# Performance work log

Hardware: AMD Instinct MI355X
Metric: run time of the kernel (lower is better)

## Reference

```python
import jax, jax.numpy as jnp
import numpy as np

N = 20000
DEG = 16
E = N * DEG
IN_DIM = 512
OUT_DIM = 512
H = 4
D = OUT_DIM // H            # head_dim = 128
POS_DIM = 3
M_ROPE = D // (POS_DIM * 2) # 21
D_ROPE = POS_DIM * 2 * M_ROPE  # 126 (2 trailing dims unrotated)
ROPE_BASE = 10000.0

INV_FREQ = jnp.exp(-jnp.arange(M_ROPE, dtype=jnp.float32) * (np.log(ROPE_BASE) / M_ROPE))


def _rope(t, pos):
    # t: (N, D, H), pos: (N, POS_DIM)
    n = t.shape[0]
    angles = pos[:, :, None] * INV_FREQ[None, None, :]        # (N, POS_DIM, M)
    cos = jnp.cos(angles)[..., None]                           # (N, POS_DIM, M, 1)
    sin = jnp.sin(angles)[..., None]
    part = t[:, :D_ROPE, :].reshape(n, POS_DIM, M_ROPE, 2, H)
    even, odd = part[..., 0, :], part[..., 1, :]
    rot_even = even * cos - odd * sin
    rot_odd = even * sin + odd * cos
    rot = jnp.stack((rot_even, rot_odd), axis=3).reshape(n, D_ROPE, H)
    return jnp.concatenate([rot, t[:, D_ROPE:, :]], axis=1)


def setup_inputs() -> dict:
    key = jax.random.key(0)
    ks = jax.random.split(key, 12)
    x = jax.random.normal(ks[0], (N, IN_DIM), jnp.float32)
    pos = jax.random.uniform(ks[1], (N, POS_DIM), jnp.float32) * 100.0
    rows = jnp.repeat(jnp.arange(N, dtype=jnp.int32), DEG)  # sorted, every node has DEG out-edges
    cols = jax.random.randint(ks[2], (E,), 0, N, dtype=jnp.int32)
    s = 1.0 / np.sqrt(IN_DIM)
    Wq = jax.random.normal(ks[3], (OUT_DIM, IN_DIM), jnp.float32) * s
    Wk = jax.random.normal(ks[4], (OUT_DIM, IN_DIM), jnp.float32) * s
    Wv = jax.random.normal(ks[5], (OUT_DIM, IN_DIM), jnp.float32) * s
    Wo = jax.random.normal(ks[6], (OUT_DIM, OUT_DIM), jnp.float32) * s
    bq = jax.random.normal(ks[7], (OUT_DIM,), jnp.float32) * 0.01
    bk = jax.random.normal(ks[8], (OUT_DIM,), jnp.float32) * 0.01
    bv = jax.random.normal(ks[9], (OUT_DIM,), jnp.float32) * 0.01
    bo = jax.random.normal(ks[10], (OUT_DIM,), jnp.float32) * 0.01
    return {"x": x, "pos": pos, "rows": rows, "cols": cols,
            "Wq": Wq, "bq": bq, "Wk": Wk, "bk": bk, "Wv": Wv, "bv": bv, "Wo": Wo, "bo": bo}


def reference(x, pos, rows, cols, Wq, bq, Wk, bk, Wv, bv, Wo, bo):
    n = x.shape[0]
    q = (x @ Wq.T + bq).reshape(n, D, H)
    k = (x @ Wk.T + bk).reshape(n, D, H)
    v = (x @ Wv.T + bv).reshape(n, D, H)
    # scaling by sqrt(k.size(1)) == sqrt(head_dim)
    q = q / jnp.sqrt(jnp.asarray(D, q.dtype))
    q = _rope(q, pos)
    k = _rope(k, pos)
    # per-edge scores: s[e,h] = sum_d q[rows[e],d,h] * k[cols[e],d,h]
    scores = jnp.einsum('edh,edh->eh', q[rows], k[cols])  # (E, H)
    # row-wise sparse softmax per head
    row_max = jax.ops.segment_max(scores, rows, num_segments=n, indices_are_sorted=True)
    p = jnp.exp(scores - row_max[rows])
    denom = jax.ops.segment_sum(p, rows, num_segments=n, indices_are_sorted=True)
    attn = p / denom[rows]                                 # (E, H)
    # bspmm: y[i,d,h] = sum_{e: rows[e]=i} attn[e,h] * v[cols[e],d,h]
    y = jax.ops.segment_sum(attn[:, None, :] * v[cols], rows, num_segments=n, indices_are_sorted=True)
    out = y.reshape(n, OUT_DIM) @ Wo.T + bo
    return out
```

## Files before the change

### kernel.cpp

```cpp
#include <hip/hip_runtime.h>
#include <hip/hip_bf16.h>

#define NN 20000
#define DEG 16
#define KD 512
#define OD 512
#define NH 4
#define DH 128
#define DROPE 126

#define BM 128
#define BN 128

typedef unsigned short u16;
typedef unsigned int u32;
typedef __attribute__((ext_vector_type(8))) short short8;
typedef __attribute__((ext_vector_type(4))) float f32x4;

__device__ __forceinline__ float b2f(u16 u){ return __uint_as_float((u32)u << 16); }
__device__ __forceinline__ u16 f2b(float f){
  u32 x = __float_as_uint(f);
  return (u16)((x + 0x7fffu + ((x >> 16) & 1u)) >> 16);
}
__device__ __forceinline__ void up8(uint4 u, float* f){
  f[0]=__uint_as_float(u.x<<16); f[1]=__uint_as_float(u.x&0xffff0000u);
  f[2]=__uint_as_float(u.y<<16); f[3]=__uint_as_float(u.y&0xffff0000u);
  f[4]=__uint_as_float(u.z<<16); f[5]=__uint_as_float(u.z&0xffff0000u);
  f[6]=__uint_as_float(u.w<<16); f[7]=__uint_as_float(u.w&0xffff0000u);
}
__device__ __forceinline__ uint4 cvt8(const float* s){
  uint4 a = *(const uint4*)s;
  uint4 b = *(const uint4*)(s + 4);
  uint4 o;
  o.x = (u32)f2b(__uint_as_float(a.x)) | ((u32)f2b(__uint_as_float(a.y)) << 16);
  o.y = (u32)f2b(__uint_as_float(a.z)) | ((u32)f2b(__uint_as_float(a.w)) << 16);
  o.z = (u32)f2b(__uint_as_float(b.x)) | ((u32)f2b(__uint_as_float(b.y)) << 16);
  o.w = (u32)f2b(__uint_as_float(b.z)) | ((u32)f2b(__uint_as_float(b.w)) << 16);
  return o;
}

__device__ __forceinline__ void load_lds16(const u16* g, u16* l) {
  __builtin_amdgcn_global_load_lds(
      (const __attribute__((address_space(1))) void*)g,
      (__attribute__((address_space(3))) void*)l, 16, 0, 0);
}

struct ConvJob {
  const float* x;  u16* xb;
  const float* w[4]; u16* wb[4];
  const float* b[4]; u16* bb[4];
};
__global__ __launch_bounds__(256) void conv_all(ConvJob j) {
  const int b = blockIdx.x;
  if (b < 5000) {
    const int i8 = (b * 256 + threadIdx.x) * 8;
    *(uint4*)(j.xb + i8) = cvt8(j.x + i8);
  } else if (b < 5512) {
    const int t = b - 5000;
    const int wsel = t >> 7;
    const int i8 = ((t & 127) * 256 + threadIdx.x) * 8;
    if (wsel < 3) {
      *(uint4*)(j.wb[wsel] + i8) = cvt8(j.w[wsel] + i8);
    } else {
      const int o = i8 >> 9, cp = i8 & 511;
      const int h = cp >> 7, d0 = cp & 127;
      const float* src = j.w[3] + (size_t)o * 512 + h;
      float tmp[8];
      #pragma unroll
      for (int t2 = 0; t2 < 8; t2++) tmp[t2] = src[(size_t)(d0 + t2) * 4];
      uint4 ov;
      ov.x = (u32)f2b(tmp[0]) | ((u32)f2b(tmp[1]) << 16);
      ov.y = (u32)f2b(tmp[2]) | ((u32)f2b(tmp[3]) << 16);
      ov.z = (u32)f2b(tmp[4]) | ((u32)f2b(tmp[5]) << 16);
      ov.w = (u32)f2b(tmp[6]) | ((u32)f2b(tmp[7]) << 16);
      *(uint4*)(j.wb[3] + i8) = ov;
    }
  } else {
    const int vsel = threadIdx.x >> 6;
    const int i8 = (threadIdx.x & 63) * 8;
    *(uint4*)(j.bb[vsel] + i8) = cvt8(j.b[vsel] + i8);
  }
}

#define BN2 256
__global__ __launch_bounds__(512, 4) void gemm_k(
    const u16* __restrict__ A,
    const u16* __restrict__ W0, const u16* __restrict__ B0,
    const u16* __restrict__ W1, const u16* __restrict__ B1,
    const u16* __restrict__ W2, const u16* __restrict__ B2,
    const float* __restrict__ pos,
    u16* __restrict__ o0, u16* __restrict__ o1, u16* __restrict__ o2,
    int M)
{
  __shared__ __align__(16) char smem[69632];
  __shared__ float posS[BM*3];
  __shared__ float freqS[21];
  u16* As = (u16*)smem;
  u16* Bs = As + BM*64;

  const int b = blockIdx.x;
  const int xcd = b & 7, rem = b >> 3;
  const int rowT = (rem / 6)*8 + xcd;
  const int sub = rem % 6;
  const int colT = sub & 1, w = sub >> 1;
  if (rowT*BM >= M) return;

  const int tid = threadIdx.x;
  const int wave = tid >> 6, lane = tid & 63;
  const int wr = wave >> 2, wc = wave & 3;
  const int lm = lane & 15, lq = lane >> 4;
  const u16* W  = (w == 0) ? W0 : ((w == 1) ? W1 : W2);
  const u16* Bi = (w == 0) ? B0 : ((w == 1) ? B1 : B2);
  const int emode = w;
  u16* outQKV = (w == 0) ? o0 : ((w == 1) ? o1 : o2);

  f32x4 acc[4][4];
  #pragma unroll
  for (int i = 0; i < 4; i++)
    #pragma unroll
    for (int jj = 0; jj < 4; jj++)
      acc[i][jj] = (f32x4){0.f, 0.f, 0.f, 0.f};

  if (emode < 2) {
    if (tid < BM) {
      int gr = rowT*BM + tid; if (gr >= M) gr = M - 1;
      posS[tid*3+0] = pos[gr*3+0];
      posS[tid*3+1] = pos[gr*3+1];
      posS[tid*3+2] = pos[gr*3+2];
    }
    if (tid >= BM && tid < BM + 21)
      freqS[tid - BM] = __expf(-(float)(tid - BM) * 0.43858763676077064f);
  }

  for (int kt = 0; kt < KD; kt += 64) {
    #pragma unroll
    for (int it = 0; it < 2; it++) {
      const int chunk = it*512 + tid;
      const int row = chunk >> 3, gseg = (chunk & 7) ^ (row & 7);
      int gr = rowT*BM + row; if (gr >= M) gr = M - 1;
      load_lds16(A + (size_t)gr*KD + kt + gseg*8,
                 As + (size_t)(it*512 + wave*64)*8);
    }
    #pragma unroll
    for (int it = 0; it < 4; it++) {
      const int chunk = it*512 + tid;
      const int row = chunk >> 3, gseg = (chunk & 7) ^ (row & 7);
      load_lds16(W + (size_t)(colT*BN2 + row)*KD + kt + gseg*8,
                 Bs + (size_t)(it*512 + wave*64)*8);
    }
    __syncthreads();
    #pragma unroll
    for (int kk = 0; kk < 64; kk += 32) {
      const int ks = kk >> 3;
      short8 af[4], bfr[4];
      #pragma unroll
      for (int i = 0; i < 4; i++) {
        const int ra = wr*64 + i*16 + lm;
        af[i] = *(const short8*)(As + (size_t)(ra*8 + ((ks + lq) ^ (ra & 7)))*8);
      }
      #pragma unroll
      for (int i = 0; i < 4; i++) {
        const int rb = wc*64 + i*16 + lm;
        bfr[i] = *(const short8*)(Bs + (size_t)(rb*8 + ((ks + lq) ^ (rb & 7)))*8);
      }
      #pragma unroll
      for (int mi = 0; mi < 4; mi++)
        #pragma unroll
        for (int ni = 0; ni < 4; ni++)
          acc[mi][ni] = __builtin_amdgcn_mfma_f32_16x16x32_bf16(af[mi], bfr[ni], acc[mi][ni], 0, 0, 0);
    }
    __syncthreads();
  }

  float bvv[4];
  #pragma unroll
  for (int ni = 0; ni < 4; ni++)
    bvv[ni] = b2f(Bi[colT*BN2 + wc*64 + ni*16 + lm]);

  u16* Cs = (u16*)smem;

  #pragma unroll
  for (int mi = 0; mi < 4; mi++) {
    #pragma unroll
    for (int ni = 0; ni < 4; ni++) {
      const int cloc = wc*64 + ni*16 + lm;
      const int h = cloc & 3, dloc = cloc >> 2;
      const int d = colT*64 + dloc;
      #pragma unroll
      for (int r = 0; r < 4; r++) {
        const int rloc = wr*64 + mi*16 + lq*4 + r;
        float v = acc[mi][ni][r] + bvv[ni];
        if (emode == 0) v *= 0.08838834764831845f;
        float vr = v;
        if (emode < 2) {
          const float partner = __shfl_xor(v, 4);
          if (d < DROPE) {
            const int pp = d / 42, rem2 = d - pp*42, m = rem2 >> 1, par = rem2 & 1;
            const float ang = posS[rloc*3 + pp] * freqS[m];
            float sn, cs; __sincosf(ang, &sn, &cs);
            vr = par ? (v*cs + partner*sn) : (v*cs - partner*sn);
          }
        }
        Cs[rloc*272 + h*68 + dloc] = f2b(vr);
      }
    }
  }
  __syncthreads();
  #pragma unroll
  for (int pass = 0; pass < 8; pass++) {
    const int c2 = pass*512 + tid;
    const int dd8 = c2 & 7, h = (c2 >> 3) & 3, rloc = c2 >> 5;
    const int grow = rowT*BM + rloc;
    if (grow < M) {
      uint2 a = *(const uint2*)(Cs + rloc*272 + h*68 + dd8*8);
      uint2 b2 = *(const uint2*)(Cs + rloc*272 + h*68 + dd8*8 + 4);
      *(uint4*)(outQKV + ((size_t)grow*NH + h)*DH + colT*64 + dd8*8)
          = make_uint4(a.x, a.y, b2.x, b2.y);
    }
  }
}

__global__ __launch_bounds__(256, 4) void gemm_o(
    const u16* __restrict__ A, const u16* __restrict__ W,
    const u16* __restrict__ Bi, float* __restrict__ out, int M)
{
  __shared__ __align__(16) u16 As[BM*64];
  __shared__ __align__(16) u16 Bs[BN*64];

  const int b = blockIdx.x;
  const int xcd = b & 7, rem = b >> 3;
  const int rowT = (rem >> 2)*8 + xcd, colT = rem & 3;
  if (rowT*BM >= M) return;

  const int tid = threadIdx.x;
  const int wave = tid >> 6, lane = tid & 63;
  const int wr = wave >> 1, wc = wave & 1;
  const int lm = lane & 15, lq = lane >> 4;

  f32x4 acc[4][4];
  #pragma unroll
  for (int i = 0; i < 4; i++)
    #pragma unroll
    for (int jj = 0; jj < 4; jj++)
      acc[i][jj] = (f32x4){0.f, 0.f, 0.f, 0.f};

  for (int kt = 0; kt < KD; kt += 64) {
    #pragma unroll
    for (int it = 0; it < 4; it++) {
      const int chunk = it*256 + wave*64 + lane;
      const int row = chunk >> 3, gseg = (chunk & 7) ^ (row & 7);
      int gr = rowT*BM + row; if (gr >= M) gr = M - 1;
      load_lds16(A + (size_t)gr*KD + kt + gseg*8,
                 As + (size_t)(it*256 + wave*64)*8);
    }
    #pragma unroll
    for (int it = 0; it < 4; it++) {
      const int chunk = it*256 + wave*64 + lane;
      const int row = chunk >> 3, gseg = (chunk & 7) ^ (row & 7);
      load_lds16(W + (size_t)(colT*BN + row)*KD + kt + gseg*8,
                 Bs + (size_t)(it*256 + wave*64)*8);
    }
    __syncthreads();
    #pragma unroll
    for (int kk = 0; kk < 64; kk += 32) {
      const int ks = kk >> 3;
      short8 af[4], bfr[4];
      #pragma unroll
      for (int i = 0; i < 4; i++) {
        const int ra = wr*64 + i*16 + lm;
        af[i] = *(const short8*)(As + (size_t)(ra*8 + ((ks + lq) ^ (ra & 7)))*8);
      }
      #pragma unroll
      for (int i = 0; i < 4; i++) {
        const int rb = wc*64 + i*16 + lm;
        bfr[i] = *(const short8*)(Bs + (size_t)(rb*8 + ((ks + lq) ^ (rb & 7)))*8);
      }
      #pragma unroll
      for (int mi = 0; mi < 4; mi++)
        #pragma unroll
        for (int ni = 0; ni < 4; ni++)
          acc[mi][ni] = __builtin_amdgcn_mfma_f32_16x16x32_bf16(af[mi], bfr[ni], acc[mi][ni], 0, 0, 0);
    }
    __syncthreads();
  }

  float bvv[4];
  #pragma unroll
  for (int ni = 0; ni < 4; ni++)
    bvv[ni] = b2f(Bi[colT*BN + wc*64 + ni*16 + lm]);

  #pragma unroll
  for (int mi = 0; mi < 4; mi++)
    #pragma unroll
    for (int ni = 0; ni < 4; ni++) {
      const int Cg = colT*BN + wc*64 + ni*16 + lm;
      #pragma unroll
      for (int r = 0; r < 4; r++) {
        const int grow = rowT*BM + wr*64 + mi*16 + lq*4 + r;
        if (grow < M) out[(size_t)grow*OD + Cg] = acc[mi][ni][r] + bvv[ni];
      }
    }
}


__global__ __launch_bounds__(256, 3) void edge_score(
    const int* __restrict__ cols, const u16* __restrict__ qf,
    const u16* __restrict__ kf, float* __restrict__ aw)
{
  const int b = blockIdx.x;
  const int xcd = b & 7;
  const int head = xcd >> 1;
  const int nbase = (b >> 3) * 32 + (xcd & 1) * 16;
  const int wave = threadIdx.x >> 6, lane = threadIdx.x & 63;
  const int g = lane >> 4, l16 = lane & 15;
  const int n = nbase + wave*4 + g;

  const int col = cols[n*DEG + l16];
  const uint4 qv = *(const uint4*)(qf + ((size_t)n*NH + head)*DH + l16*8);

  uint4 kreg[16];
  #pragma unroll
  for (int jj = 0; jj < 16; jj++) {
    const int cj = __shfl(col, g*16 + jj);
    kreg[jj] = *(const uint4*)(kf + ((size_t)cj*NH + head)*DH + l16*8);
  }
  float qa[8]; up8(qv, qa);

  float s = 0.f;
  #pragma unroll
  for (int jj = 0; jj < 16; jj++) {
    float ka[8]; up8(kreg[jj], ka);
    float pr = qa[0]*ka[0] + qa[1]*ka[1] + qa[2]*ka[2] + qa[3]*ka[3]
             + qa[4]*ka[4] + qa[5]*ka[5] + qa[6]*ka[6] + qa[7]*ka[7];
    pr += __shfl_xor(pr, 1);
    pr += __shfl_xor(pr, 2);
    pr += __shfl_xor(pr, 4);
    pr += __shfl_xor(pr, 8);
    s = (l16 == jj) ? pr : s;
  }

  float mx = s;
  #pragma unroll
  for (int msk = 1; msk < 16; msk <<= 1) mx = fmaxf(mx, __shfl_xor(mx, msk));
  float p = expf(s - mx);
  float dn = p;
  #pragma unroll
  for (int msk = 1; msk < 16; msk <<= 1) dn += __shfl_xor(dn, msk);
  aw[(size_t)(n*NH + head)*DEG + l16] = p / dn;
}

__global__ __launch_bounds__(256, 3) void edge_gather(
    const int* __restrict__ cols, const u16* __restrict__ vf,
    const float* __restrict__ aw, u16* __restrict__ y)
{
  const int b = blockIdx.x;
  const int xcd = b & 7;
  const int head = xcd >> 1;
  const int nbase = (b >> 3) * 32 + (xcd & 1) * 16;
  const int wave = threadIdx.x >> 6, lane = threadIdx.x & 63;
  const int g = lane >> 4, l16 = lane & 15;
  const int n = nbase + wave*4 + g;

  const int col = cols[n*DEG + l16];
  const float a_l = aw[(size_t)(n*NH + head)*DEG + l16];

  uint4 vreg[16];
  #pragma unroll
  for (int jj = 0; jj < 16; jj++) {
    const int cj = __shfl(col, g*16 + jj);
    vreg[jj] = *(const uint4*)(vf + ((size_t)cj*NH + head)*DH + l16*8);
  }

  float ya[8];
  #pragma unroll
  for (int t = 0; t < 8; t++) ya[t] = 0.f;
  #pragma unroll
  for (int jj = 0; jj < 16; jj++) {
    const float a = __shfl(a_l, g*16 + jj);
    float va[8]; up8(vreg[jj], va);
    #pragma unroll
    for (int t = 0; t < 8; t++) ya[t] += a*va[t];
  }
  u32 pk[4];
  #pragma unroll
  for (int t = 0; t < 4; t++)
    pk[t] = (u32)f2b(ya[2*t]) | ((u32)f2b(ya[2*t+1]) << 16);
  *(uint4*)(y + ((size_t)n*NH + head)*DH + l16*8) = make_uint4(pk[0], pk[1], pk[2], pk[3]);
}

extern "C" void kernel_launch(void* const* d_in, const int* in_sizes, int n_in,
                              void* d_out, int out_size, void* d_ws, size_t ws_size,
                              hipStream_t stream) {
  (void)in_sizes; (void)n_in; (void)out_size; (void)ws_size;
  const float* x   = (const float*)d_in[0];
  const float* pos = (const float*)d_in[1];
  const int* cols = (const int*)d_in[3];
  const float* Wq = (const float*)d_in[4];
  const float* bq = (const float*)d_in[5];
  const float* Wk = (const float*)d_in[6];
  const float* bk = (const float*)d_in[7];
  const float* Wv = (const float*)d_in[8];
  const float* bv = (const float*)d_in[9];
  const float* Wo = (const float*)d_in[10];
  const float* bo = (const float*)d_in[11];

  char* ws = (char*)d_ws;
  size_t off = 0;
  auto carve = [&](size_t bytes) { char* p = ws + off; off += (bytes + 15) & ~(size_t)15; return p; };
  u16* xb   = (u16*)carve((size_t)NN*KD*2);
  u16* Wqb  = (u16*)carve((size_t)OD*KD*2);
  u16* Wkb  = (u16*)carve((size_t)OD*KD*2);
  u16* Wvb  = (u16*)carve((size_t)OD*KD*2);
  u16* Wob  = (u16*)carve((size_t)OD*OD*2);
  u16* bqb  = (u16*)carve((size_t)OD*2);
  u16* bkb  = (u16*)carve((size_t)OD*2);
  u16* bvb  = (u16*)carve((size_t)OD*2);
  u16* bob  = (u16*)carve((size_t)OD*2);
  u16* qf   = (u16*)carve((size_t)NN*OD*2);
  u16* kf   = (u16*)carve((size_t)NN*OD*2);
  u16* vf   = (u16*)carve((size_t)NN*OD*2);
  u16* y    = (u16*)carve((size_t)NN*OD*2);
  float* aw = (float*)carve((size_t)NN*NH*DEG*4);

  ConvJob cj;
  cj.x = x; cj.xb = xb;
  cj.w[0]=Wq; cj.w[1]=Wk; cj.w[2]=Wv; cj.w[3]=Wo;
  cj.wb[0]=Wqb; cj.wb[1]=Wkb; cj.wb[2]=Wvb; cj.wb[3]=Wob;
  cj.b[0]=bq; cj.b[1]=bk; cj.b[2]=bv; cj.b[3]=bo;
  cj.bb[0]=bqb; cj.bb[1]=bkb; cj.bb[2]=bvb; cj.bb[3]=bob;
  conv_all<<<dim3(5513), 256, 0, stream>>>(cj);

  gemm_k<<<dim3(960), 512, 0, stream>>>(xb, Wqb, bqb, Wkb, bkb, Wvb, bvb, pos,
                                        qf, kf, vf, NN);
  edge_score<<<dim3(5000), 256, 0, stream>>>(cols, qf, kf, aw);
  edge_gather<<<dim3(5000), 256, 0, stream>>>(cols, vf, aw, y);
  gemm_o<<<dim3(640), 256, 0, stream>>>(y, Wob, bob, (float*)d_out, NN);
}
```

Baseline: 231.5 us.

## Shrink gemm_k LDS via two-phase epilogue and widen gemm_o tiles to 128x256

The QKV GEMM epilogue now stages output through LDS in two 64-row halves, which cuts the shared buffer from 68KB to 48KB and raises the launch-bounds occupancy target to 6. The output-projection GEMM moves to 512-thread blocks with 128x256 tiles, halving the grid and reusing each A tile across more columns. The aim is better latency hiding and less redundant A traffic. The trade-offs are an extra barrier in the epilogue and possible register pressure under the tighter launch bounds.

```diff
diff --git a/kernel.cpp b/kernel.cpp
--- a/kernel.cpp
+++ b/kernel.cpp
@@ -10,7 +10,7 @@
 #define DROPE 126
 
 #define BM 128
-#define BN 128
+#define BN2 256
 
 typedef unsigned short u16;
 typedef unsigned int u32;
@@ -82,8 +82,7 @@
   }
 }
 
-#define BN2 256
-__global__ __launch_bounds__(512, 4) void gemm_k(
+__global__ __launch_bounds__(512, 6) void gemm_k(
     const u16* __restrict__ A,
     const u16* __restrict__ W0, const u16* __restrict__ B0,
     const u16* __restrict__ W1, const u16* __restrict__ B1,
@@ -92,7 +91,7 @@
     u16* __restrict__ o0, u16* __restrict__ o1, u16* __restrict__ o2,
     int M)
 {
-  __shared__ __align__(16) char smem[69632];
+  __shared__ __align__(16) char smem[49152];
   __shared__ float posS[BM*3];
   __shared__ float freqS[21];
   u16* As = (u16*)smem;
@@ -180,61 +179,67 @@
   u16* Cs = (u16*)smem;
 
   #pragma unroll
-  for (int mi = 0; mi < 4; mi++) {
-    #pragma unroll
-    for (int ni = 0; ni < 4; ni++) {
-      const int cloc = wc*64 + ni*16 + lm;
-      const int h = cloc & 3, dloc = cloc >> 2;
-      const int d = colT*64 + dloc;
-      #pragma unroll
-      for (int r = 0; r < 4; r++) {
-        const int rloc = wr*64 + mi*16 + lq*4 + r;
-        float v = acc[mi][ni][r] + bvv[ni];
-        if (emode == 0) v *= 0.08838834764831845f;
-        float vr = v;
-        if (emode < 2) {
-          const float partner = __shfl_xor(v, 4);
-          if (d < DROPE) {
-            const int pp = d / 42, rem2 = d - pp*42, m = rem2 >> 1, par = rem2 & 1;
-            const float ang = posS[rloc*3 + pp] * freqS[m];
-            float sn, cs; __sincosf(ang, &sn, &cs);
-            vr = par ? (v*cs + partner*sn) : (v*cs - partner*sn);
+  for (int ph = 0; ph < 2; ph++) {
+    if (ph) __syncthreads();
+    if (wr == ph) {
+      #pragma unroll
+      for (int mi = 0; mi < 4; mi++) {
+        #pragma unroll
+        for (int ni = 0; ni < 4; ni++) {
+          const int cloc = wc*64 + ni*16 + lm;
+          const int h = cloc & 3, dloc = cloc >> 2;
+          const int d = colT*64 + dloc;
+          #pragma unroll
+          for (int r = 0; r < 4; r++) {
+            const int rl = mi*16 + lq*4 + r;
+            float v = acc[mi][ni][r] + bvv[ni];
+            if (emode == 0) v *= 0.08838834764831845f;
+            float vr = v;
+            if (emode < 2) {
+              const float partner = __shfl_xor(v, 4);
+              if (d < DROPE) {
+                const int pp = d / 42, rem2 = d - pp*42, m = rem2 >> 1, par = rem2 & 1;
+                const float ang = posS[(ph*64 + rl)*3 + pp] * freqS[m];
+                float sn, cs; __sincosf(ang, &sn, &cs);
+                vr = par ? (v*cs + partner*sn) : (v*cs - partner*sn);
+              }
+            }
+            Cs[rl*272 + h*68 + dloc] = f2b(vr);
           }
         }
-        Cs[rloc*272 + h*68 + dloc] = f2b(vr);
-      }
-    }
-  }
-  __syncthreads();
-  #pragma unroll
-  for (int pass = 0; pass < 8; pass++) {
-    const int c2 = pass*512 + tid;
-    const int dd8 = c2 & 7, h = (c2 >> 3) & 3, rloc = c2 >> 5;
-    const int grow = rowT*BM + rloc;
-    if (grow < M) {
-      uint2 a = *(const uint2*)(Cs + rloc*272 + h*68 + dd8*8);
-      uint2 b2 = *(const uint2*)(Cs + rloc*272 + h*68 + dd8*8 + 4);
-      *(uint4*)(outQKV + ((size_t)grow*NH + h)*DH + colT*64 + dd8*8)
-          = make_uint4(a.x, a.y, b2.x, b2.y);
-    }
-  }
-}
-
-__global__ __launch_bounds__(256, 4) void gemm_o(
+      }
+    }
+    __syncthreads();
+    #pragma unroll
+    for (int pass = 0; pass < 4; pass++) {
+      const int c2 = pass*512 + tid;
+      const int dd8 = c2 & 7, h = (c2 >> 3) & 3, rl = c2 >> 5;
+      const int grow = rowT*BM + ph*64 + rl;
+      if (grow < M) {
+        uint2 a = *(const uint2*)(Cs + rl*272 + h*68 + dd8*8);
+        uint2 b2 = *(const uint2*)(Cs + rl*272 + h*68 + dd8*8 + 4);
+        *(uint4*)(outQKV + ((size_t)grow*NH + h)*DH + colT*64 + dd8*8)
+            = make_uint4(a.x, a.y, b2.x, b2.y);
+      }
+    }
+  }
+}
+
+__global__ __launch_bounds__(512, 6) void gemm_o(
     const u16* __restrict__ A, const u16* __restrict__ W,
     const u16* __restrict__ Bi, float* __restrict__ out, int M)
 {
   __shared__ __align__(16) u16 As[BM*64];
-  __shared__ __align__(16) u16 Bs[BN*64];
+  __shared__ __align__(16) u16 Bs[BN2*64];
 
   const int b = blockIdx.x;
   const int xcd = b & 7, rem = b >> 3;
-  const int rowT = (rem >> 2)*8 + xcd, colT = rem & 3;
+  const int rowT = (rem >> 1)*8 + xcd, colT = rem & 1;
   if (rowT*BM >= M) return;
 
   const int tid = threadIdx.x;
   const int wave = tid >> 6, lane = tid & 63;
-  const int wr = wave >> 1, wc = wave & 1;
+  const int wr = wave >> 2, wc = wave & 3;
   const int lm = lane & 15, lq = lane >> 4;
 
   f32x4 acc[4][4];
@@ -246,19 +251,19 @@
 
   for (int kt = 0; kt < KD; kt += 64) {
     #pragma unroll
-    for (int it = 0; it < 4; it++) {
-      const int chunk = it*256 + wave*64 + lane;
+    for (int it = 0; it < 2; it++) {
+      const int chunk = it*512 + tid;
       const int row = chunk >> 3, gseg = (chunk & 7) ^ (row & 7);
       int gr = rowT*BM + row; if (gr >= M) gr = M - 1;
       load_lds16(A + (size_t)gr*KD + kt + gseg*8,
-                 As + (size_t)(it*256 + wave*64)*8);
+                 As + (size_t)(it*512 + wave*64)*8);
     }
     #pragma unroll
     for (int it = 0; it < 4; it++) {
-      const int chunk = it*256 + wave*64 + lane;
+      const int chunk = it*512 + tid;
       const int row = chunk >> 3, gseg = (chunk & 7) ^ (row & 7);
-      load_lds16(W + (size_t)(colT*BN + row)*KD + kt + gseg*8,
-                 Bs + (size_t)(it*256 + wave*64)*8);
+      load_lds16(W + (size_t)(colT*BN2 + row)*KD + kt + gseg*8,
+                 Bs + (size_t)(it*512 + wave*64)*8);
     }
     __syncthreads();
     #pragma unroll
@@ -287,13 +292,13 @@
   float bvv[4];
   #pragma unroll
   for (int ni = 0; ni < 4; ni++)
-    bvv[ni] = b2f(Bi[colT*BN + wc*64 + ni*16 + lm]);
+    bvv[ni] = b2f(Bi[colT*BN2 + wc*64 + ni*16 + lm]);
 
   #pragma unroll
   for (int mi = 0; mi < 4; mi++)
     #pragma unroll
     for (int ni = 0; ni < 4; ni++) {
-      const int Cg = colT*BN + wc*64 + ni*16 + lm;
+      const int Cg = colT*BN2 + wc*64 + ni*16 + lm;
       #pragma unroll
       for (int r = 0; r < 4; r++) {
         const int grow = rowT*BM + wr*64 + mi*16 + lq*4 + r;
@@ -434,5 +439,5 @@
                                         qf, kf, vf, NN);
   edge_score<<<dim3(5000), 256, 0, stream>>>(cols, qf, kf, aw);
   edge_gather<<<dim3(5000), 256, 0, stream>>>(cols, vf, aw, y);
-  gemm_o<<<dim3(640), 256, 0, stream>>>(y, Wob, bob, (float*)d_out, NN);
-}
+  gemm_o<<<dim3(320), 512, 0, stream>>>(y, Wob, bob, (float*)d_out, NN);
+}
```

Measured after the change: 491.7 us. +112.4%, slower.
